# Kernel optimization log

Hardware: AMD Instinct MI355X
Metric: run time of the kernel (lower is better)

## Reference

```python
import jax, jax.numpy as jnp
import numpy as np

N = 50000      # nodes
E = 800000     # edges (before self-loops)
IN_DIM = 128
HID = 96
PROJ = 64
BN_EPS = 1e-5
L2_EPS = 1e-12


def setup_inputs() -> dict:
    key = jax.random.key(0)
    ks = jax.random.split(key, 8)

    def glorot(k, shape):
        fan_in, fan_out = shape
        s = np.sqrt(6.0 / (fan_in + fan_out)).astype(np.float32)
        return jax.random.uniform(k, shape, jnp.float32, -s, s)

    x = jax.random.normal(ks[0], (N, IN_DIM), jnp.float32)
    edge_index = jax.random.randint(ks[1], (2, E), 0, N, dtype=jnp.int64)

    return {
        "x": x,
        "edge_index": edge_index,
        # GCN layer 1
        "W1": glorot(ks[2], (IN_DIM, HID)), "b1": jnp.zeros(HID, jnp.float32),
        "g1": jnp.ones(HID, jnp.float32), "be1": jnp.zeros(HID, jnp.float32),
        # GCN layer 2
        "W2": glorot(ks[3], (HID, HID)), "b2": jnp.zeros(HID, jnp.float32),
        "g2": jnp.ones(HID, jnp.float32), "be2": jnp.zeros(HID, jnp.float32),
        # projector: Linear -> BN -> ReLU -> Linear
        "Wp1": glorot(ks[4], (HID, HID)), "bp1": jnp.zeros(HID, jnp.float32),
        "gp": jnp.ones(HID, jnp.float32), "bep": jnp.zeros(HID, jnp.float32),
        "Wp2": glorot(ks[5], (HID, PROJ)), "bp2": jnp.zeros(PROJ, jnp.float32),
    }


def _batchnorm(h, gamma, beta):
    # training-mode BatchNorm1d: batch stats, biased variance
    m = h.mean(axis=0)
    v = h.var(axis=0)
    return gamma * (h - m) * jax.lax.rsqrt(v + BN_EPS) + beta


def _gcn_conv(x, W, b, src, dst, deg_inv_sqrt):
    # PyG GCNConv: x @ W, symmetric-normalized scatter-add (self-loops included
    # in src/dst), then bias.
    xw = x @ W                                              # [N, out]
    norm = deg_inv_sqrt[src] * deg_inv_sqrt[dst]            # [E+N]
    msg = xw[src] * norm[:, None]                           # [E+N, out]
    out = jax.ops.segment_sum(msg, dst, num_segments=x.shape[0])
    return out + b


def reference(x, edge_index, W1, b1, g1, be1, W2, b2, g2, be2,
              Wp1, bp1, gp, bep, Wp2, bp2):
    n = x.shape[0]
    loops = jnp.arange(n, dtype=edge_index.dtype)
    src = jnp.concatenate([edge_index[0], loops])
    dst = jnp.concatenate([edge_index[1], loops])
    deg = jax.ops.segment_sum(jnp.ones(src.shape[0], x.dtype), dst,
                              num_segments=n)               # includes self-loops
    deg_inv_sqrt = jax.lax.rsqrt(deg)                       # deg >= 1 always

    h = jax.nn.relu(_batchnorm(_gcn_conv(x, W1, b1, src, dst, deg_inv_sqrt), g1, be1))
    h = jax.nn.relu(_batchnorm(_gcn_conv(h, W2, b2, src, dst, deg_inv_sqrt), g2, be2))

    z = jax.nn.relu(_batchnorm(h @ Wp1 + bp1, gp, bep))
    z = z @ Wp2 + bp2
    # F.normalize(p=2, dim=-1, eps=1e-12)
    nrm = jnp.linalg.norm(z, axis=-1, keepdims=True)
    return z / jnp.maximum(nrm, L2_EPS)
```

## Files before the change

kernel.cpp:

```cpp
#include <hip/hip_runtime.h>
#include <hip/hip_fp16.h>

constexpr int BLK = 256;

static inline int cdiv(long long a, int b) { return (int)((a + b - 1) / b); }

using v8h = __attribute__((ext_vector_type(8))) _Float16;
using v4f = __attribute__((ext_vector_type(4))) float;


__global__ void zero_int(int* __restrict__ p, int n) {
    for (int i = blockIdx.x * blockDim.x + threadIdx.x; i < n; i += gridDim.x * blockDim.x)
        p[i] = 0;
}


__global__ void count_dst_off(const int* __restrict__ dst, int* __restrict__ cnt,
                              int* __restrict__ eoff, int E) {
    for (int i = blockIdx.x * blockDim.x + threadIdx.x; i < E; i += gridDim.x * blockDim.x)
        eoff[i] = atomicAdd(&cnt[dst[i]], 1);
}

__global__ void scan1_dis(const int* __restrict__ cnt, int* __restrict__ rowptr,
                          int* __restrict__ bsum, float* __restrict__ dis, int N) {
    __shared__ int ts[256];
    int tid = threadIdx.x;
    int base = blockIdx.x * 1024 + tid * 4;
    int v[4], s = 0;
#pragma unroll
    for (int i = 0; i < 4; ++i) {
        v[i] = (base + i < N) ? cnt[base + i] : 0;
        s += v[i];
        if (base + i < N) dis[base + i] = rsqrtf((float)v[i] + 1.0f);
    }
    ts[tid] = s;
    __syncthreads();
    for (int off = 1; off < 256; off <<= 1) {
        int t = 0;
        if (tid >= off) t = ts[tid - off];
        __syncthreads();
        if (tid >= off) ts[tid] += t;
        __syncthreads();
    }
    int run = ts[tid] - s;
#pragma unroll
    for (int i = 0; i < 4; ++i) {
        if (base + i < N) rowptr[base + i] = run;
        run += v[i];
    }
    if (tid == 255) bsum[blockIdx.x] = ts[255];
}

__global__ void scan2z(const int* __restrict__ bsum, int* __restrict__ boff, int nb,
                       float* __restrict__ sums) {
    int tid = threadIdx.x;
    if (tid < 64) {
        int orig = (tid < nb) ? bsum[tid] : 0;
        int v = orig;
#pragma unroll
        for (int off = 1; off < 64; off <<= 1) {
            int t = __shfl_up(v, off, 64);
            if (tid >= off) v += t;
        }
        if (tid < nb) boff[tid] = v - orig;
    } else if (tid < 64 + 576) {
        sums[tid - 64] = 0.0f;
    }
}

__global__ void scan3(int* __restrict__ rowptr, const int* __restrict__ boff, int N, int E) {
    int i = blockIdx.x * blockDim.x + threadIdx.x;
    if (i < N) rowptr[i] += boff[i >> 10];
    if (i == 0) rowptr[N] = E;
}

__global__ void csr_fill(const int* __restrict__ src, const int* __restrict__ dst,
                         const int* __restrict__ eoff, const int* __restrict__ rowptr,
                         int* __restrict__ csrc, int E) {
    for (int i = blockIdx.x * blockDim.x + threadIdx.x; i < E; i += gridDim.x * blockDim.x) {
        csrc[rowptr[dst[i]] + eoff[i]] = src[i];
    }
}


template <int K, bool ACT, bool BIAS, bool HOUT, bool WOUT>
__global__ __launch_bounds__(256) void gemm96m(const float* __restrict__ in,
                                               const float* __restrict__ W,
                                               const float* __restrict__ bias,
                                               const float* __restrict__ ss,
                                               float* __restrict__ out,
                                               _Float16* __restrict__ hout, int N) {
    constexpr int NK = K / 32;
    constexpr int LDK = K + 8;
    __shared__ __align__(16) _Float16 Wt[96 * LDK];
    const int tid = threadIdx.x;
    for (int idx = tid; idx < K * 96; idx += 256) {
        int k = idx / 96, n = idx - k * 96;
        Wt[n * LDK + k] = (_Float16)W[idx];
    }
    __syncthreads();

    const int wave = tid >> 6, lane = tid & 63;
    const int quad = lane >> 4, lm = lane & 15;
    const int rbase = blockIdx.x * 64 + wave * 16;
    int arow = rbase + lm;
    arow = arow < N ? arow : N - 1;

    v8h afr[NK];
#pragma unroll
    for (int kc = 0; kc < NK; ++kc) {
        const float* p = &in[(long long)arow * K + kc * 32 + quad * 8];
        float4 p0 = *(const float4*)p;
        float4 p1 = *(const float4*)(p + 4);
        if (ACT) {
            int kk = kc * 32 + quad * 8;
            float4 sc0 = *(const float4*)&ss[kk];
            float4 sc1 = *(const float4*)&ss[kk + 4];
            float4 sh0 = *(const float4*)&ss[96 + kk];
            float4 sh1 = *(const float4*)&ss[96 + kk + 4];
            p0.x = fmaxf(fmaf(p0.x, sc0.x, sh0.x), 0.0f);
            p0.y = fmaxf(fmaf(p0.y, sc0.y, sh0.y), 0.0f);
            p0.z = fmaxf(fmaf(p0.z, sc0.z, sh0.z), 0.0f);
            p0.w = fmaxf(fmaf(p0.w, sc0.w, sh0.w), 0.0f);
            p1.x = fmaxf(fmaf(p1.x, sc1.x, sh1.x), 0.0f);
            p1.y = fmaxf(fmaf(p1.y, sc1.y, sh1.y), 0.0f);
            p1.z = fmaxf(fmaf(p1.z, sc1.z, sh1.z), 0.0f);
            p1.w = fmaxf(fmaf(p1.w, sc1.w, sh1.w), 0.0f);
        }
        v8h a;
        a[0] = (_Float16)p0.x; a[1] = (_Float16)p0.y;
        a[2] = (_Float16)p0.z; a[3] = (_Float16)p0.w;
        a[4] = (_Float16)p1.x; a[5] = (_Float16)p1.y;
        a[6] = (_Float16)p1.z; a[7] = (_Float16)p1.w;
        afr[kc] = a;
    }

    v4f acc[6];
#pragma unroll
    for (int t = 0; t < 6; ++t) {
        v4f c = {0.0f, 0.0f, 0.0f, 0.0f};
#pragma unroll
        for (int kc = 0; kc < NK; ++kc) {
            v8h b = *(const v8h*)&Wt[(t * 16 + lm) * LDK + kc * 32 + quad * 8];
            c = __builtin_amdgcn_mfma_f32_16x16x32_f16(afr[kc], b, c, 0, 0, 0);
        }
        acc[t] = c;
    }

#pragma unroll
    for (int t = 0; t < 6; ++t) {
        float bv = BIAS ? bias[t * 16 + lm] : 0.0f;
#pragma unroll
        for (int r = 0; r < 4; ++r) {
            int gr = rbase + quad * 4 + r;
            if (gr < N) {
                float o = acc[t][r] + bv;
                if (WOUT) out[(long long)gr * 96 + t * 16 + lm] = o;
                if (HOUT) hout[(long long)gr * 96 + t * 16 + lm] = (_Float16)o;
            }
        }
    }
}


__global__ __launch_bounds__(256) void gemm_finalm(const float* __restrict__ in,
                                                   const float* __restrict__ W,
                                                   const float* __restrict__ bias,
                                                   const float* __restrict__ ss,
                                                   float* __restrict__ out, int N) {
    constexpr int K = 96, NK = 3, LDK = K + 8;
    __shared__ __align__(16) _Float16 Wt[64 * LDK];
    const int tid = threadIdx.x;
    for (int idx = tid; idx < K * 64; idx += 256) {
        int k = idx / 64, n = idx - k * 64;
        Wt[n * LDK + k] = (_Float16)W[idx];
    }
    __syncthreads();

    const int wave = tid >> 6, lane = tid & 63;
    const int quad = lane >> 4, lm = lane & 15;
    const int rbase = blockIdx.x * 64 + wave * 16;
    int arow = rbase + lm;
    arow = arow < N ? arow : N - 1;

    v8h afr[NK];
#pragma unroll
    for (int kc = 0; kc < NK; ++kc) {
        const float* p = &in[(long long)arow * K + kc * 32 + quad * 8];
        float4 p0 = *(const float4*)p;
        float4 p1 = *(const float4*)(p + 4);
        int kk = kc * 32 + quad * 8;
        float4 sc0 = *(const float4*)&ss[kk];
        float4 sc1 = *(const float4*)&ss[kk + 4];
        float4 sh0 = *(const float4*)&ss[96 + kk];
        float4 sh1 = *(const float4*)&ss[96 + kk + 4];
        p0.x = fmaxf(fmaf(p0.x, sc0.x, sh0.x), 0.0f);
        p0.y = fmaxf(fmaf(p0.y, sc0.y, sh0.y), 0.0f);
        p0.z = fmaxf(fmaf(p0.z, sc0.z, sh0.z), 0.0f);
        p0.w = fmaxf(fmaf(p0.w, sc0.w, sh0.w), 0.0f);
        p1.x = fmaxf(fmaf(p1.x, sc1.x, sh1.x), 0.0f);
        p1.y = fmaxf(fmaf(p1.y, sc1.y, sh1.y), 0.0f);
        p1.z = fmaxf(fmaf(p1.z, sc1.z, sh1.z), 0.0f);
        p1.w = fmaxf(fmaf(p1.w, sc1.w, sh1.w), 0.0f);
        v8h a;
        a[0] = (_Float16)p0.x; a[1] = (_Float16)p0.y;
        a[2] = (_Float16)p0.z; a[3] = (_Float16)p0.w;
        a[4] = (_Float16)p1.x; a[5] = (_Float16)p1.y;
        a[6] = (_Float16)p1.z; a[7] = (_Float16)p1.w;
        afr[kc] = a;
    }

    v4f acc[4];
#pragma unroll
    for (int t = 0; t < 4; ++t) {
        v4f c = {0.0f, 0.0f, 0.0f, 0.0f};
#pragma unroll
        for (int kc = 0; kc < NK; ++kc) {
            v8h b = *(const v8h*)&Wt[(t * 16 + lm) * LDK + kc * 32 + quad * 8];
            c = __builtin_amdgcn_mfma_f32_16x16x32_f16(afr[kc], b, c, 0, 0, 0);
        }
        float bv = bias[t * 16 + lm];
        c[0] += bv; c[1] += bv; c[2] += bv; c[3] += bv;
        acc[t] = c;
    }

    float sq[4];
#pragma unroll
    for (int r = 0; r < 4; ++r) {
        float s = acc[0][r] * acc[0][r] + acc[1][r] * acc[1][r] +
                  acc[2][r] * acc[2][r] + acc[3][r] * acc[3][r];
#pragma unroll
        for (int m = 1; m < 16; m <<= 1) s += __shfl_xor(s, m, 64);
        sq[r] = 1.0f / fmaxf(sqrtf(s), 1e-12f);
    }
#pragma unroll
    for (int r = 0; r < 4; ++r) {
        int gr = rbase + quad * 4 + r;
        if (gr < N) {
#pragma unroll
            for (int t = 0; t < 4; ++t)
                out[(long long)gr * 64 + t * 16 + lm] = acc[t][r] * sq[r];
        }
    }
}


__global__ __launch_bounds__(256) void agg96h(const __half* __restrict__ hxw,
                                              const int* __restrict__ rowptr,
                                              const int* __restrict__ csrc,
                                              const float* __restrict__ dis,
                                              const float* __restrict__ bias,
                                              float* __restrict__ out, int N) {
    int idx = blockIdx.x * 256 + threadIdx.x;
    if (idx >= N * 12) return;
    int n = idx / 12, c8 = idx % 12;
    float dn = dis[n];
    float acc[8];
    {
        float dd = dn * dn;
        float4 g = *(const float4*)&hxw[(long long)n * 96 + c8 * 8];
        const __half2* hs = (const __half2*)&g;
#pragma unroll
        for (int k = 0; k < 4; ++k) {
            float2 f = __half22float2(hs[k]);
            acc[2 * k + 0] = fmaf(f.x, dd, bias[c8 * 8 + 2 * k + 0]);
            acc[2 * k + 1] = fmaf(f.y, dd, bias[c8 * 8 + 2 * k + 1]);
        }
    }
    int e = rowptr[n], e1 = rowptr[n + 1];
    for (; e + 3 < e1; e += 4) {
        int s0 = csrc[e], s1 = csrc[e + 1], s2 = csrc[e + 2], s3 = csrc[e + 3];
        float w0 = dis[s0] * dn, w1 = dis[s1] * dn, w2 = dis[s2] * dn, w3 = dis[s3] * dn;
        float4 g0 = *(const float4*)&hxw[(long long)s0 * 96 + c8 * 8];
        float4 g1 = *(const float4*)&hxw[(long long)s1 * 96 + c8 * 8];
        float4 g2 = *(const float4*)&hxw[(long long)s2 * 96 + c8 * 8];
        float4 g3 = *(const float4*)&hxw[(long long)s3 * 96 + c8 * 8];
        const __half2* h0 = (const __half2*)&g0;
        const __half2* h1 = (const __half2*)&g1;
        const __half2* h2 = (const __half2*)&g2;
        const __half2* h3 = (const __half2*)&g3;
#pragma unroll
        for (int k = 0; k < 4; ++k) {
            float2 f0 = __half22float2(h0[k]);
            float2 f1 = __half22float2(h1[k]);
            float2 f2 = __half22float2(h2[k]);
            float2 f3 = __half22float2(h3[k]);
            acc[2 * k + 0] = fmaf(f0.x, w0, acc[2 * k + 0]);
            acc[2 * k + 1] = fmaf(f0.y, w0, acc[2 * k + 1]);
            acc[2 * k + 0] = fmaf(f1.x, w1, acc[2 * k + 0]);
            acc[2 * k + 1] = fmaf(f1.y, w1, acc[2 * k + 1]);
            acc[2 * k + 0] = fmaf(f2.x, w2, acc[2 * k + 0]);
            acc[2 * k + 1] = fmaf(f2.y, w2, acc[2 * k + 1]);
            acc[2 * k + 0] = fmaf(f3.x, w3, acc[2 * k + 0]);
            acc[2 * k + 1] = fmaf(f3.y, w3, acc[2 * k + 1]);
        }
    }
    for (; e < e1; ++e) {
        int s0 = csrc[e];
        float w0 = dis[s0] * dn;
        float4 g0 = *(const float4*)&hxw[(long long)s0 * 96 + c8 * 8];
        const __half2* h0 = (const __half2*)&g0;
#pragma unroll
        for (int k = 0; k < 4; ++k) {
            float2 f0 = __half22float2(h0[k]);
            acc[2 * k + 0] = fmaf(f0.x, w0, acc[2 * k + 0]);
            acc[2 * k + 1] = fmaf(f0.y, w0, acc[2 * k + 1]);
        }
    }
    float4 o0, o1;
    o0.x = acc[0]; o0.y = acc[1]; o0.z = acc[2]; o0.w = acc[3];
    o1.x = acc[4]; o1.y = acc[5]; o1.z = acc[6]; o1.w = acc[7];
    *(float4*)&out[(long long)n * 96 + c8 * 8] = o0;
    *(float4*)&out[(long long)n * 96 + c8 * 8 + 4] = o1;
}


__global__ __launch_bounds__(256) void bn_stats96(const float* __restrict__ h,
                                                  float* __restrict__ sums, int N) {
    __shared__ float sb[192];
    const int tid = threadIdx.x;
    if (tid < 192) sb[tid] = 0.0f;
    __syncthreads();
    int g = blockIdx.x * 256 + tid;
    int total = N * 24, stride = gridDim.x * 256;
    float4 s4 = {0, 0, 0, 0}, q4 = {0, 0, 0, 0};
    int c4 = g % 24;
    for (int i = g; i < total; i += stride) {
        int n = i / 24;
        float4 v = *(const float4*)&h[n * 96 + 4 * c4];
        s4.x += v.x; s4.y += v.y; s4.z += v.z; s4.w += v.w;
        q4.x += v.x * v.x; q4.y += v.y * v.y; q4.z += v.z * v.z; q4.w += v.w * v.w;
    }
    atomicAdd(&sb[4 * c4 + 0], s4.x);
    atomicAdd(&sb[4 * c4 + 1], s4.y);
    atomicAdd(&sb[4 * c4 + 2], s4.z);
    atomicAdd(&sb[4 * c4 + 3], s4.w);
    atomicAdd(&sb[96 + 4 * c4 + 0], q4.x);
    atomicAdd(&sb[96 + 4 * c4 + 1], q4.y);
    atomicAdd(&sb[96 + 4 * c4 + 2], q4.z);
    atomicAdd(&sb[96 + 4 * c4 + 3], q4.w);
    __syncthreads();
    if (tid < 192) atomicAdd(&sums[tid], sb[tid]);
}

__global__ void bn_finalize96(const float* __restrict__ sums, const float* __restrict__ gamma,
                              const float* __restrict__ beta, float* __restrict__ ss, int N) {
    int i = threadIdx.x;
    if (i < 96) {
        float inv_n = 1.0f / (float)N;
        float mean = sums[i] * inv_n;
        float var = sums[96 + i] * inv_n - mean * mean;
        float sc = gamma[i] * rsqrtf(var + 1e-5f);
        ss[i] = sc;
        ss[96 + i] = beta[i] - mean * sc;
    }
}


extern "C" void kernel_launch(void* const* d_in, const int* in_sizes, int n_in,
                              void* d_out, int out_size, void* d_ws, size_t ws_size,
                              hipStream_t stream) {
    const float* x   = (const float*)d_in[0];
    const int*   ei  = (const int*)d_in[1];
    const float* W1  = (const float*)d_in[2];
    const float* b1  = (const float*)d_in[3];
    const float* g1  = (const float*)d_in[4];
    const float* be1 = (const float*)d_in[5];
    const float* W2  = (const float*)d_in[6];
    const float* b2  = (const float*)d_in[7];
    const float* g2  = (const float*)d_in[8];
    const float* be2 = (const float*)d_in[9];
    const float* Wp1 = (const float*)d_in[10];
    const float* bp1 = (const float*)d_in[11];
    const float* gp  = (const float*)d_in[12];
    const float* bep = (const float*)d_in[13];
    const float* Wp2 = (const float*)d_in[14];
    const float* bp2 = (const float*)d_in[15];

    const int N = in_sizes[0] / 128;
    const int E = in_sizes[1] / 2;
    const int* src = ei;
    const int* dst = ei + E;

    char* w = (char*)d_ws;
    auto alloc = [&](size_t bytes) { char* p = w; w += (bytes + 15) & ~size_t(15); return p; };
    int*      cnt    = (int*)alloc((size_t)N * 4);
    int*      rowptr = (int*)alloc((size_t)(N + 1) * 4);
    int*      bsum   = (int*)alloc(64 * 4);
    int*      boff   = (int*)alloc(64 * 4);
    float*    dis    = (float*)alloc((size_t)N * 4);
    int*      eoff   = (int*)alloc((size_t)E * 4);
    int*      csrc   = (int*)alloc((size_t)E * 4);
    float*    buf1   = (float*)alloc((size_t)N * 96 * 4);
    float*    buf2   = (float*)alloc((size_t)N * 96 * 4);
    _Float16* hbuf   = (_Float16*)alloc((size_t)N * 96 * 2);
    float*    sums   = (float*)alloc(576 * 4);
    float*    ss     = (float*)alloc(576 * 4);
    float* sums1 = sums, *sums2 = sums + 192, *sums3 = sums + 384;
    float* ss1 = ss, *ss2 = ss + 192, *ss3 = ss + 384;

    float* out = (float*)d_out;

    const int gE  = cdiv(E, BLK);
    const int gG  = cdiv(N, 64);
    const int gA  = cdiv((long long)N * 12, BLK);
    const int nb  = cdiv(N, 1024);

    zero_int<<<cdiv(N, BLK), BLK, 0, stream>>>(cnt, N);
    count_dst_off<<<gE, BLK, 0, stream>>>(dst, cnt, eoff, E);
    scan1_dis<<<nb, 256, 0, stream>>>(cnt, rowptr, bsum, dis, N);
    scan2z<<<1, 640, 0, stream>>>(bsum, boff, nb, sums);
    scan3<<<cdiv(N, BLK), BLK, 0, stream>>>(rowptr, boff, N, E);
    csr_fill<<<gE, BLK, 0, stream>>>(src, dst, eoff, rowptr, csrc, E);

    gemm96m<128, false, false, true, false><<<gG, 256, 0, stream>>>(x, W1, nullptr, nullptr,
                                                                    nullptr, hbuf, N);
    agg96h<<<gA, 256, 0, stream>>>((const __half*)hbuf, rowptr, csrc, dis, b1, buf2, N);
    bn_stats96<<<512, 256, 0, stream>>>(buf2, sums1, N);
    bn_finalize96<<<1, 128, 0, stream>>>(sums1, g1, be1, ss1, N);

    gemm96m<96, true, false, true, false><<<gG, 256, 0, stream>>>(buf2, W2, nullptr, ss1,
                                                                  nullptr, hbuf, N);
    agg96h<<<gA, 256, 0, stream>>>((const __half*)hbuf, rowptr, csrc, dis, b2, buf2, N);
    bn_stats96<<<512, 256, 0, stream>>>(buf2, sums2, N);
    bn_finalize96<<<1, 128, 0, stream>>>(sums2, g2, be2, ss2, N);

    gemm96m<96, true, true, false, true><<<gG, 256, 0, stream>>>(buf2, Wp1, bp1, ss2,
                                                                 buf1, nullptr, N);
    bn_stats96<<<512, 256, 0, stream>>>(buf1, sums3, N);
    bn_finalize96<<<1, 128, 0, stream>>>(sums3, gp, bep, ss3, N);

    gemm_finalm<<<gG, 256, 0, stream>>>(buf1, Wp2, bp2, ss3, out, N);
}
```

Measured before the change: 350.7 us.

## Fuse BN finalize into GEMM prologues and projector BN stats into GEMM epilogue

```diff
diff --git a/kernel.cpp b/kernel.cpp
--- a/kernel.cpp
+++ b/kernel.cpp
@@ -78,26 +78,40 @@
                          const int* __restrict__ eoff, const int* __restrict__ rowptr,
                          int* __restrict__ csrc, int E) {
     for (int i = blockIdx.x * blockDim.x + threadIdx.x; i < E; i += gridDim.x * blockDim.x) {
-        csrc[rowptr[dst[i]] + eoff[i]] = src[i];
-    }
-}
-
-
-template <int K, bool ACT, bool BIAS, bool HOUT, bool WOUT>
+        __builtin_nontemporal_store(src[i], &csrc[rowptr[dst[i]] + eoff[i]]);
+    }
+}
+
+
+template <int K, bool ACT, bool BIAS, bool HOUT, bool WOUT, bool STATS>
 __global__ __launch_bounds__(256) void gemm96m(const float* __restrict__ in,
                                                const float* __restrict__ W,
                                                const float* __restrict__ bias,
-                                               const float* __restrict__ ss,
+                                               const float* __restrict__ bnsums,
+                                               const float* __restrict__ gamma,
+                                               const float* __restrict__ beta,
                                                float* __restrict__ out,
-                                               _Float16* __restrict__ hout, int N) {
+                                               _Float16* __restrict__ hout,
+                                               float* __restrict__ osums, int N) {
     constexpr int NK = K / 32;
     constexpr int LDK = K + 8;
     __shared__ __align__(16) _Float16 Wt[96 * LDK];
+    __shared__ __align__(16) float ssl[ACT ? 192 : 1];
+    __shared__ float sb[STATS ? 192 : 1];
     const int tid = threadIdx.x;
     for (int idx = tid; idx < K * 96; idx += 256) {
         int k = idx / 96, n = idx - k * 96;
         Wt[n * LDK + k] = (_Float16)W[idx];
     }
+    if (ACT && tid < 96) {
+        float inv_n = 1.0f / (float)N;
+        float mean = bnsums[tid] * inv_n;
+        float var = bnsums[96 + tid] * inv_n - mean * mean;
+        float sc = gamma[tid] * rsqrtf(var + 1e-5f);
+        ssl[tid] = sc;
+        ssl[96 + tid] = beta[tid] - mean * sc;
+    }
+    if (STATS && tid < 192) sb[tid] = 0.0f;
     __syncthreads();
 
     const int wave = tid >> 6, lane = tid & 63;
@@ -114,10 +128,10 @@
         float4 p1 = *(const float4*)(p + 4);
         if (ACT) {
             int kk = kc * 32 + quad * 8;
-            float4 sc0 = *(const float4*)&ss[kk];
-            float4 sc1 = *(const float4*)&ss[kk + 4];
-            float4 sh0 = *(const float4*)&ss[96 + kk];
-            float4 sh1 = *(const float4*)&ss[96 + kk + 4];
+            float4 sc0 = *(const float4*)&ssl[kk];
+            float4 sc1 = *(const float4*)&ssl[kk + 4];
+            float4 sh0 = *(const float4*)&ssl[96 + kk];
+            float4 sh1 = *(const float4*)&ssl[96 + kk + 4];
             p0.x = fmaxf(fmaf(p0.x, sc0.x, sh0.x), 0.0f);
             p0.y = fmaxf(fmaf(p0.y, sc0.y, sh0.y), 0.0f);
             p0.z = fmaxf(fmaf(p0.z, sc0.z, sh0.z), 0.0f);
@@ -147,6 +161,9 @@
         acc[t] = c;
     }
 
+    float ls[6], lq[6];
+#pragma unroll
+    for (int t = 0; t < 6; ++t) { ls[t] = 0.0f; lq[t] = 0.0f; }
 #pragma unroll
     for (int t = 0; t < 6; ++t) {
         float bv = BIAS ? bias[t * 16 + lm] : 0.0f;
@@ -157,8 +174,27 @@
                 float o = acc[t][r] + bv;
                 if (WOUT) out[(long long)gr * 96 + t * 16 + lm] = o;
                 if (HOUT) hout[(long long)gr * 96 + t * 16 + lm] = (_Float16)o;
+                if (STATS) { ls[t] += o; lq[t] += o * o; }
             }
         }
+    }
+    if (STATS) {
+#pragma unroll
+        for (int t = 0; t < 6; ++t) {
+            ls[t] += __shfl_xor(ls[t], 16);
+            ls[t] += __shfl_xor(ls[t], 32);
+            lq[t] += __shfl_xor(lq[t], 16);
+            lq[t] += __shfl_xor(lq[t], 32);
+        }
+        if (quad == 0) {
+#pragma unroll
+            for (int t = 0; t < 6; ++t) {
+                atomicAdd(&sb[t * 16 + lm], ls[t]);
+                atomicAdd(&sb[96 + t * 16 + lm], lq[t]);
+            }
+        }
+        __syncthreads();
+        if (tid < 192) atomicAdd(&osums[tid], sb[tid]);
     }
 }
 
@@ -166,14 +202,25 @@
 __global__ __launch_bounds__(256) void gemm_finalm(const float* __restrict__ in,
                                                    const float* __restrict__ W,
                                                    const float* __restrict__ bias,
-                                                   const float* __restrict__ ss,
+                                                   const float* __restrict__ bnsums,
+                                                   const float* __restrict__ gamma,
+                                                   const float* __restrict__ beta,
                                                    float* __restrict__ out, int N) {
     constexpr int K = 96, NK = 3, LDK = K + 8;
     __shared__ __align__(16) _Float16 Wt[64 * LDK];
+    __shared__ __align__(16) float ssl[192];
     const int tid = threadIdx.x;
     for (int idx = tid; idx < K * 64; idx += 256) {
         int k = idx / 64, n = idx - k * 64;
         Wt[n * LDK + k] = (_Float16)W[idx];
+    }
+    if (tid < 96) {
+        float inv_n = 1.0f / (float)N;
+        float mean = bnsums[tid] * inv_n;
+        float var = bnsums[96 + tid] * inv_n - mean * mean;
+        float sc = gamma[tid] * rsqrtf(var + 1e-5f);
+        ssl[tid] = sc;
+        ssl[96 + tid] = beta[tid] - mean * sc;
     }
     __syncthreads();
 
@@ -190,10 +237,10 @@
         float4 p0 = *(const float4*)p;
         float4 p1 = *(const float4*)(p + 4);
         int kk = kc * 32 + quad * 8;
-        float4 sc0 = *(const float4*)&ss[kk];
-        float4 sc1 = *(const float4*)&ss[kk + 4];
-        float4 sh0 = *(const float4*)&ss[96 + kk];
-        float4 sh1 = *(const float4*)&ss[96 + kk + 4];
+        float4 sc0 = *(const float4*)&ssl[kk];
+        float4 sc1 = *(const float4*)&ssl[kk + 4];
+        float4 sh0 = *(const float4*)&ssl[96 + kk];
+        float4 sh1 = *(const float4*)&ssl[96 + kk + 4];
         p0.x = fmaxf(fmaf(p0.x, sc0.x, sh0.x), 0.0f);
         p0.y = fmaxf(fmaf(p0.y, sc0.y, sh0.y), 0.0f);
         p0.z = fmaxf(fmaf(p0.z, sc0.z, sh0.z), 0.0f);
@@ -268,31 +315,48 @@
         }
     }
     int e = rowptr[n], e1 = rowptr[n + 1];
+    for (; e + 7 < e1; e += 8) {
+        int s[8];
+        float w[8];
+        float4 g[8];
+#pragma unroll
+        for (int j = 0; j < 8; ++j) s[j] = csrc[e + j];
+#pragma unroll
+        for (int j = 0; j < 8; ++j) w[j] = dis[s[j]] * dn;
+#pragma unroll
+        for (int j = 0; j < 8; ++j)
+            g[j] = *(const float4*)&hxw[(long long)s[j] * 96 + c8 * 8];
+#pragma unroll
+        for (int j = 0; j < 8; ++j) {
+            const __half2* h = (const __half2*)&g[j];
+#pragma unroll
+            for (int k = 0; k < 4; ++k) {
+                float2 f = __half22float2(h[k]);
+                acc[2 * k + 0] = fmaf(f.x, w[j], acc[2 * k + 0]);
+                acc[2 * k + 1] = fmaf(f.y, w[j], acc[2 * k + 1]);
+            }
+        }
+    }
     for (; e + 3 < e1; e += 4) {
-        int s0 = csrc[e], s1 = csrc[e + 1], s2 = csrc[e + 2], s3 = csrc[e + 3];
-        float w0 = dis[s0] * dn, w1 = dis[s1] * dn, w2 = dis[s2] * dn, w3 = dis[s3] * dn;
-        float4 g0 = *(const float4*)&hxw[(long long)s0 * 96 + c8 * 8];
-        float4 g1 = *(const float4*)&hxw[(long long)s1 * 96 + c8 * 8];
-        float4 g2 = *(const float4*)&hxw[(long long)s2 * 96 + c8 * 8];
-        float4 g3 = *(const float4*)&hxw[(long long)s3 * 96 + c8 * 8];
-        const __half2* h0 = (const __half2*)&g0;
-        const __half2* h1 = (const __half2*)&g1;
-        const __half2* h2 = (const __half2*)&g2;
-        const __half2* h3 = (const __half2*)&g3;
-#pragma unroll
-        for (int k = 0; k < 4; ++k) {
-            float2 f0 = __half22float2(h0[k]);
-            float2 f1 = __half22float2(h1[k]);
-            float2 f2 = __half22float2(h2[k]);
-            float2 f3 = __half22float2(h3[k]);
-            acc[2 * k + 0] = fmaf(f0.x, w0, acc[2 * k + 0]);
-            acc[2 * k + 1] = fmaf(f0.y, w0, acc[2 * k + 1]);
-            acc[2 * k + 0] = fmaf(f1.x, w1, acc[2 * k + 0]);
-            acc[2 * k + 1] = fmaf(f1.y, w1, acc[2 * k + 1]);
-            acc[2 * k + 0] = fmaf(f2.x, w2, acc[2 * k + 0]);
-            acc[2 * k + 1] = fmaf(f2.y, w2, acc[2 * k + 1]);
-            acc[2 * k + 0] = fmaf(f3.x, w3, acc[2 * k + 0]);
-            acc[2 * k + 1] = fmaf(f3.y, w3, acc[2 * k + 1]);
+        int s[4];
+        float w[4];
+        float4 g[4];
+#pragma unroll
+        for (int j = 0; j < 4; ++j) s[j] = csrc[e + j];
+#pragma unroll
+        for (int j = 0; j < 4; ++j) w[j] = dis[s[j]] * dn;
+#pragma unroll
+        for (int j = 0; j < 4; ++j)
+            g[j] = *(const float4*)&hxw[(long long)s[j] * 96 + c8 * 8];
+#pragma unroll
+        for (int j = 0; j < 4; ++j) {
+            const __half2* h = (const __half2*)&g[j];
+#pragma unroll
+            for (int k = 0; k < 4; ++k) {
+                float2 f = __half22float2(h[k]);
+                acc[2 * k + 0] = fmaf(f.x, w[j], acc[2 * k + 0]);
+                acc[2 * k + 1] = fmaf(f.y, w[j], acc[2 * k + 1]);
+            }
         }
     }
     for (; e < e1; ++e) {
@@ -341,19 +405,6 @@
     atomicAdd(&sb[96 + 4 * c4 + 3], q4.w);
     __syncthreads();
     if (tid < 192) atomicAdd(&sums[tid], sb[tid]);
-}
-
-__global__ void bn_finalize96(const float* __restrict__ sums, const float* __restrict__ gamma,
-                              const float* __restrict__ beta, float* __restrict__ ss, int N) {
-    int i = threadIdx.x;
-    if (i < 96) {
-        float inv_n = 1.0f / (float)N;
-        float mean = sums[i] * inv_n;
-        float var = sums[96 + i] * inv_n - mean * mean;
-        float sc = gamma[i] * rsqrtf(var + 1e-5f);
-        ss[i] = sc;
-        ss[96 + i] = beta[i] - mean * sc;
-    }
 }
 
 
@@ -395,9 +446,7 @@
     float*    buf2   = (float*)alloc((size_t)N * 96 * 4);
     _Float16* hbuf   = (_Float16*)alloc((size_t)N * 96 * 2);
     float*    sums   = (float*)alloc(576 * 4);
-    float*    ss     = (float*)alloc(576 * 4);
     float* sums1 = sums, *sums2 = sums + 192, *sums3 = sums + 384;
-    float* ss1 = ss, *ss2 = ss + 192, *ss3 = ss + 384;
 
     float* out = (float*)d_out;
 
@@ -413,22 +462,18 @@
     scan3<<<cdiv(N, BLK), BLK, 0, stream>>>(rowptr, boff, N, E);
     csr_fill<<<gE, BLK, 0, stream>>>(src, dst, eoff, rowptr, csrc, E);
 
-    gemm96m<128, false, false, true, false><<<gG, 256, 0, stream>>>(x, W1, nullptr, nullptr,
-                                                                    nullptr, hbuf, N);
+    gemm96m<128, false, false, true, false, false><<<gG, 256, 0, stream>>>(
+        x, W1, nullptr, nullptr, nullptr, nullptr, nullptr, hbuf, nullptr, N);
     agg96h<<<gA, 256, 0, stream>>>((const __half*)hbuf, rowptr, csrc, dis, b1, buf2, N);
     bn_stats96<<<512, 256, 0, stream>>>(buf2, sums1, N);
-    bn_finalize96<<<1, 128, 0, stream>>>(sums1, g1, be1, ss1, N);
-
-    gemm96m<96, true, false, true, false><<<gG, 256, 0, stream>>>(buf2, W2, nullptr, ss1,
-                                                                  nullptr, hbuf, N);
+
+    gemm96m<96, true, false, true, false, false><<<gG, 256, 0, stream>>>(
+        buf2, W2, nullptr, sums1, g1, be1, nullptr, hbuf, nullptr, N);
     agg96h<<<gA, 256, 0, stream>>>((const __half*)hbuf, rowptr, csrc, dis, b2, buf2, N);
     bn_stats96<<<512, 256, 0, stream>>>(buf2, sums2, N);
-    bn_finalize96<<<1, 128, 0, stream>>>(sums2, g2, be2, ss2, N);
-
-    gemm96m<96, true, true, false, true><<<gG, 256, 0, stream>>>(buf2, Wp1, bp1, ss2,
-                                                                 buf1, nullptr, N);
-    bn_stats96<<<512, 256, 0, stream>>>(buf1, sums3, N);
-    bn_finalize96<<<1, 128, 0, stream>>>(sums3, gp, bep, ss3, N);
-
-    gemm_finalm<<<gG, 256, 0, stream>>>(buf1, Wp2, bp2, ss3, out, N);
-}
+
+    gemm96m<96, true, true, false, true, true><<<gG, 256, 0, stream>>>(
+        buf2, Wp1, bp1, sums2, g2, be2, buf1, nullptr, sums3, N);
+
+    gemm_finalm<<<gG, 256, 0, stream>>>(buf1, Wp2, bp2, sums3, gp, bep, out, N);
+}
```

New measurement: 353.1 us. About the same (+0.7%).
